# Kernel tuning notes

Measured on AMD Instinct MI355X. Metric: run time of the kernel, lower is better.

## Reference

```python
import jax, jax.numpy as jnp
import numpy as np

P, N, D = 8, 1024, 768
H = 12
HS = D // H
SCALE = float(HS ** 0.5)  # NOTE: original multiplies by sqrt(head_size)


def setup_inputs() -> dict:
    key = jax.random.key(0)
    k1, k2, k3 = jax.random.split(key, 3)
    pixel_values = jax.random.normal(k1, (P, N, D), dtype=jnp.float32)
    attention_mask = jnp.zeros((P, 1, 1, N), dtype=jnp.float32)
    qkv_w = jax.random.normal(k2, (D, 3 * D), dtype=jnp.float32) * 0.02
    qkv_b = jnp.zeros((3 * D,), dtype=jnp.float32)
    proj_w = jax.random.normal(k3, (D, D), dtype=jnp.float32) * 0.02
    proj_b = jnp.zeros((D,), dtype=jnp.float32)
    return {
        "pixel_values": pixel_values,
        "attention_mask": attention_mask,
        "qkv_w": qkv_w,
        "qkv_b": qkv_b,
        "proj_w": proj_w,
        "proj_b": proj_b,
    }


def reference(pixel_values, attention_mask, qkv_w, qkv_b, proj_w, proj_b):
    p, n, d = pixel_values.shape
    # fused QKV projection: (p, n, 3d) -> (3, p, H, n, hs)
    mixed = pixel_values @ qkv_w + qkv_b
    mixed = mixed.reshape(p, n, 3, H, HS).transpose(2, 0, 3, 1, 4)
    q, k, v = mixed[0], mixed[1], mixed[2]
    # scores: (p, H, n, n); original multiplies by sqrt(head_size)
    scores = jnp.einsum("phqd,phkd->phqk", q, k) * SCALE
    probs = jax.nn.softmax(scores, axis=-1)
    # dropout p=0 (identity in eval); mask added POST-softmax, per source
    probs = probs + attention_mask
    ctx = jnp.einsum("phqk,phkd->phqd", probs, v)
    ctx = ctx.transpose(0, 2, 1, 3).reshape(p, n, d)
    out = ctx @ proj_w + proj_b
    return out
```

## Files before the change

### kernel.cpp

```cpp
#include <hip/hip_runtime.h>
#include <hip/hip_bf16.h>
#include <cstdint>
#include <math.h>

constexpr int PB = 8;
constexpr int NS = 1024;
constexpr int DM = 768;
constexpr int NH = 12;
constexpr int HSZ = 64;
constexpr float QS    = 11.541560327111707f;
constexpr float EOFFL = 126.95716359822878f;

typedef short    bf16x8 __attribute__((ext_vector_type(8)));
typedef _Float16 half8  __attribute__((ext_vector_type(8)));
typedef __fp16   fp16x2 __attribute__((ext_vector_type(2)));
typedef float    floatx4 __attribute__((ext_vector_type(4)));

#if __has_builtin(__builtin_amdgcn_exp2f)
#define EXP2(x) __builtin_amdgcn_exp2f(x)
#else
#define EXP2(x) exp2f(x)
#endif

__device__ __forceinline__ ushort f2h(float x) {
    _Float16 h = (_Float16)x;
    return *reinterpret_cast<ushort*>(&h);
}
__device__ __forceinline__ float h2f(ushort u) {
    _Float16 h = __builtin_bit_cast(_Float16, u);
    return (float)h;
}
__device__ __forceinline__ ushort f2bf(float x) {
    __hip_bfloat16 b = __float2bfloat16(x);
    return *reinterpret_cast<ushort*>(&b);
}
__device__ __forceinline__ float bf2f(ushort u) {
    __hip_bfloat16 b = *reinterpret_cast<__hip_bfloat16*>(&u);
    return __bfloat162float(b);
}
__device__ __forceinline__ unsigned int pk2h(float a, float b) {
    fp16x2 h = __builtin_amdgcn_cvt_pkrtz(a, b);
    return __builtin_bit_cast(unsigned int, h);
}

#define GLDS(g, l)                                                             \
    __builtin_amdgcn_global_load_lds(                                          \
        (const __attribute__((address_space(1))) void*)(g),                    \
        (__attribute__((address_space(3))) void*)(l), 16, 0, 0)

__global__ void prep_kernel(const float* __restrict__ x, ushort* __restrict__ hf,
                            int n4,
                            const float* __restrict__ qkv_w, ushort* __restrict__ qwf,
                            const float* __restrict__ proj_w, ushort* __restrict__ pwf)
{
    const int bid = blockIdx.x;
    if (bid < 2048) {
        int i = bid * blockDim.x + threadIdx.x;
        const int stride = 2048 * blockDim.x;
        for (; i < n4; i += stride) {
            const float4 v = ((const float4*)x)[i];
            ((ushort4*)hf)[i] = ushort4{f2h(v.x), f2h(v.y), f2h(v.z), f2h(v.w)};
        }
        return;
    }
    __shared__ float tile[32][33];
    const int t  = threadIdx.x;
    const int tx = t & 31, ty = t >> 5;
    const float* w;
    ushort* fT;
    int bx, by, K, N;
    if (bid < 2048 + 1728) {
        const int id = bid - 2048;
        bx = id % 72; by = id / 72;
        w = qkv_w; fT = qwf; K = DM; N = 3 * DM;
    } else {
        const int id = bid - (2048 + 1728);
        bx = id % 24; by = id / 24;
        w = proj_w; fT = pwf; K = DM; N = DM;
    }
    #pragma unroll
    for (int r = 0; r < 4; ++r)
        tile[ty + r*8][tx] = w[(size_t)(by*32 + ty + r*8) * N + bx*32 + tx];
    __syncthreads();
    #pragma unroll
    for (int r = 0; r < 4; ++r) {
        const int n = bx*32 + ty + r*8;
        const int k = by*32 + tx;
        fT[(size_t)n * K + k] = f2h(tile[tx][ty + r*8]);
    }
}

template <int MODE>
__global__ __launch_bounds__(256, 3)
void gemm_f16(const ushort* __restrict__ Af, const ushort* __restrict__ Bf,
              const float* __restrict__ bias, float* __restrict__ outf,
              ushort* __restrict__ qf, ushort* __restrict__ kf,
              ushort* __restrict__ vt, int K)
{
    __shared__ __align__(16) ushort As[128*64];
    __shared__ __align__(16) ushort Bs[128*64];

    const int t    = threadIdx.x;
    const int w    = t >> 6;
    const int lane = t & 63;
    const int l15  = lane & 15;
    const int quad = lane >> 4;
    const int wm = w >> 1, wn = w & 1;
    const int m0 = blockIdx.x * 128, n0 = blockIdx.y * 128;

    floatx4 acc[4][4];
    #pragma unroll
    for (int i = 0; i < 4; ++i)
        #pragma unroll
        for (int j = 0; j < 4; ++j) acc[i][j] = floatx4{0.f, 0.f, 0.f, 0.f};

    const int srow8 = lane >> 3;
    const int sslot = lane & 7;

    for (int k0 = 0; k0 < K; k0 += 64) {
        #pragma unroll
        for (int j = 0; j < 4; ++j) {
            const int row = w*32 + j*8 + srow8;
            const int seg = sslot ^ (row & 7);
            const int ldst = (w*32 + j*8) * 64;
            GLDS(Af + (size_t)(m0 + row) * K + k0 + seg*8, As + ldst);
            GLDS(Bf + (size_t)(n0 + row) * K + k0 + seg*8, Bs + ldst);
        }
        __syncthreads();

        #pragma unroll
        for (int h2 = 0; h2 < 2; ++h2) {
            half8 fa[4], fb[4];
            #pragma unroll
            for (int i = 0; i < 4; ++i) {
                const int sl = ((h2*4 + quad) ^ (l15 & 7)) * 8;
                fa[i] = *(const half8*)(As + (wm*64 + i*16 + l15) * 64 + sl);
                fb[i] = *(const half8*)(Bs + (wn*64 + i*16 + l15) * 64 + sl);
            }
            #pragma unroll
            for (int mt = 0; mt < 4; ++mt)
                #pragma unroll
                for (int nt = 0; nt < 4; ++nt)
                    acc[mt][nt] = __builtin_amdgcn_mfma_f32_16x16x32_f16(fa[mt], fb[nt], acc[mt][nt], 0, 0, 0);
        }
        __syncthreads();
    }

    if (MODE == 0) {
        #pragma unroll
        for (int nt = 0; nt < 4; ++nt) {
            const int col = n0 + wn*64 + nt*16 + l15;
            const float bval = bias[col];
            #pragma unroll
            for (int mt = 0; mt < 4; ++mt) {
                const int row0 = m0 + wm*64 + mt*16 + quad*4;
                #pragma unroll
                for (int r = 0; r < 4; ++r)
                    outf[(size_t)(row0 + r) * DM + col] = acc[mt][nt][r] + bval;
            }
        }
    } else {
        const int jbase = n0 + wn*64;
        const int c  = jbase / DM;
        const int hh = (jbase % DM) >> 6;
        const int pp = (m0 + wm*64) >> 10;
        const size_t head = (size_t)pp * NH + hh;
        if (c < 2) {
            ushort* dst = (c == 0 ? qf : kf);
            const float qscale = (c == 0) ? QS : 1.0f;
            #pragma unroll
            for (int nt = 0; nt < 4; ++nt) {
                const int s = nt*16 + l15;
                const float bval = bias[jbase + s];
                #pragma unroll
                for (int mt = 0; mt < 4; ++mt) {
                    const int tok0 = m0 + wm*64 + mt*16 + quad*4;
                    const int nn0  = tok0 & 1023;
                    #pragma unroll
                    for (int r = 0; r < 4; ++r)
                        dst[(head*NS + nn0 + r) * HSZ + s] = f2h((acc[mt][nt][r] + bval) * qscale);
                }
            }
        } else {
            #pragma unroll
            for (int nt = 0; nt < 4; ++nt) {
                const int s = nt*16 + l15;
                const float bval = bias[jbase + s];
                #pragma unroll
                for (int mt = 0; mt < 4; ++mt) {
                    const int tok0 = m0 + wm*64 + mt*16 + quad*4;
                    const int nn0  = tok0 & 1023;
                    ushort4 pk;
                    pk.x = f2bf(acc[mt][nt][0] + bval);
                    pk.y = f2bf(acc[mt][nt][1] + bval);
                    pk.z = f2bf(acc[mt][nt][2] + bval);
                    pk.w = f2bf(acc[mt][nt][3] + bval);
                    *(ushort4*)(vt + (head*HSZ + s) * NS + nn0) = pk;
                }
            }
        }
    }
}

__global__ void mv_kernel(const float* __restrict__ mask, const ushort* __restrict__ vt,
                          float* __restrict__ mv)
{
    __shared__ float red[4][64];
    const int ph = blockIdx.x;
    const int t  = threadIdx.x;
    const int c  = t & 63, part = t >> 6;
    const ushort* vrow = vt + ((size_t)ph * HSZ + c) * NS + part * 256;
    const float*  mrow = mask + (size_t)(ph / NH) * NS + part * 256;
    float acc = 0.f;
    for (int k = 0; k < 256; k += 4) {
        const ushort4 v4 = *(const ushort4*)(vrow + k);
        const float4  m4 = *(const float4*)(mrow + k);
        acc += m4.x * bf2f(v4.x) + m4.y * bf2f(v4.y)
             + m4.z * bf2f(v4.z) + m4.w * bf2f(v4.w);
    }
    red[part][c] = acc;
    __syncthreads();
    if (t < 64)
        mv[(size_t)ph * HSZ + t] = red[0][t] + red[1][t] + red[2][t] + red[3][t];
}

__global__ __launch_bounds__(256, 3)
void attn_mfma_kernel(const ushort* __restrict__ qf, const ushort* __restrict__ kf,
                      const ushort* __restrict__ vt, const float* __restrict__ mv,
                      ushort* __restrict__ ctx)
{
    __shared__ __align__(16) ushort khs[2][64*64];
    __shared__ __align__(16) ushort vs [2][64*64];

    const int t    = threadIdx.x;
    const int w    = t >> 6;
    const int lane = t & 63;
    const int l15  = lane & 15;
    const int quad = lane >> 4;
    const int ph = blockIdx.x, qt = blockIdx.y;
    const int h  = ph % NH,    p  = ph / NH;
    const size_t headoff = ((size_t)p * NH + h) * (size_t)(NS * HSZ);

    const ushort* qpa = qf + headoff + (size_t)(qt*128 + w*16 + l15) * HSZ + quad*8;
    const half8 qa0 = *(const half8*)(qpa);
    const half8 qa1 = *(const half8*)(qpa + 32);
    const ushort* qpb = qpa + (size_t)64 * HSZ;
    const half8 qb0 = *(const half8*)(qpb);
    const half8 qb1 = *(const half8*)(qpb + 32);

    floatx4 oA[4], oB[4];
    float lsumA = 0.f, lsumB = 0.f;
    #pragma unroll
    for (int tc = 0; tc < 4; ++tc) {
        oA[tc] = floatx4{0.f, 0.f, 0.f, 0.f};
        oB[tc] = floatx4{0.f, 0.f, 0.f, 0.f};
    }

    const int srow8 = lane >> 3;
    const int sslot = lane & 7;
    const int xs = l15 & 7;

    auto stage = [&](int kt, int b) {
        #pragma unroll
        for (int j = 0; j < 2; ++j) {
            const int row  = w*16 + j*8 + srow8;
            const int segK = sslot ^ ((row & 3) | (((row >> 3) & 1) << 2));
            const int segV = sslot ^ (row & 7);
            const size_t gk = headoff + (size_t)(kt*64 + row) * HSZ + segK*8;
            const size_t gv = headoff + (size_t)row * NS + kt*64 + segV*8;
            const int ldst = (w*16 + j*8) * 64;
            GLDS(kf + gk, &khs[b][ldst]);
            GLDS(vt + gv, &vs [b][ldst]);
        }
    };

    stage(0, 0);
    int cur = 0;

    for (int kt = 0; kt < 16; ++kt) {
        __syncthreads();
        if (kt + 1 < 16) stage(kt + 1, cur ^ 1);

        const ushort* kbuf = khs[cur];
        const ushort* vbuf = vs [cur];

        bf16x8 bpA[2], bpB[2];
        #pragma unroll
        for (int tt = 0; tt < 4; ++tt) {
            const int rho = ((l15 >> 2) << 3) + ((tt & 1) << 2) + (l15 & 3) + ((tt >> 1) << 5);
            const int a0 = rho*64 + ((quad       ^ xs) * 8);
            const int a1 = rho*64 + (((quad | 4) ^ xs) * 8);
            const half8 bh0 = *(const half8*)(kbuf + a0);
            const half8 bh1 = *(const half8*)(kbuf + a1);
            floatx4 sA = floatx4{-EOFFL, -EOFFL, -EOFFL, -EOFFL};
            sA = __builtin_amdgcn_mfma_f32_16x16x32_f16(bh0, qa0, sA, 0, 0, 0);
            sA = __builtin_amdgcn_mfma_f32_16x16x32_f16(bh1, qa1, sA, 0, 0, 0);
            floatx4 sB = floatx4{-EOFFL, -EOFFL, -EOFFL, -EOFFL};
            sB = __builtin_amdgcn_mfma_f32_16x16x32_f16(bh0, qb0, sB, 0, 0, 0);
            sB = __builtin_amdgcn_mfma_f32_16x16x32_f16(bh1, qb1, sB, 0, 0, 0);
            const float a0e = EXP2(sA[0]);
            const float a1e = EXP2(sA[1]);
            const float a2e = EXP2(sA[2]);
            const float a3e = EXP2(sA[3]);
            lsumA += (a0e + a1e) + (a2e + a3e);
            const float b0e = EXP2(sB[0]);
            const float b1e = EXP2(sB[1]);
            const float b2e = EXP2(sB[2]);
            const float b3e = EXP2(sB[3]);
            lsumB += (b0e + b1e) + (b2e + b3e);
            const int off = (tt & 1) * 4;
            bf16x8& dA = bpA[tt >> 1];
            dA[off + 0] = (short)f2bf(a0e);
            dA[off + 1] = (short)f2bf(a1e);
            dA[off + 2] = (short)f2bf(a2e);
            dA[off + 3] = (short)f2bf(a3e);
            bf16x8& dB = bpB[tt >> 1];
            dB[off + 0] = (short)f2bf(b0e);
            dB[off + 1] = (short)f2bf(b1e);
            dB[off + 2] = (short)f2bf(b2e);
            dB[off + 3] = (short)f2bf(b3e);
        }

        #pragma unroll
        for (int tc = 0; tc < 4; ++tc) {
            const int crow = (tc*16 + l15) * 64;
            const bf16x8 va0 = *(const bf16x8*)(vbuf + crow + ((quad       ^ xs) * 8));
            const bf16x8 va1 = *(const bf16x8*)(vbuf + crow + (((quad | 4) ^ xs) * 8));
            oA[tc] = __builtin_amdgcn_mfma_f32_16x16x32_bf16(va0, bpA[0], oA[tc], 0, 0, 0);
            oA[tc] = __builtin_amdgcn_mfma_f32_16x16x32_bf16(va1, bpA[1], oA[tc], 0, 0, 0);
            oB[tc] = __builtin_amdgcn_mfma_f32_16x16x32_bf16(va0, bpB[0], oB[tc], 0, 0, 0);
            oB[tc] = __builtin_amdgcn_mfma_f32_16x16x32_bf16(va1, bpB[1], oB[tc], 0, 0, 0);
        }
        cur ^= 1;
    }

    float lA = lsumA;
    lA += __shfl_xor(lA, 16);
    lA += __shfl_xor(lA, 32);
    const float invA = 1.0f / lA;
    float lB = lsumB;
    lB += __shfl_xor(lB, 16);
    lB += __shfl_xor(lB, 32);
    const float invB = 1.0f / lB;

    const float* mvp = mv + ((size_t)p * NH + h) * HSZ;
    const int rowA = qt*128 + w*16 + l15;
    const size_t baseA = ((size_t)p * NS + rowA) * DM + h * 64;
    const size_t baseB = baseA + (size_t)64 * DM;
    #pragma unroll
    for (int tc = 0; tc < 4; ++tc) {
        const int c0 = tc*16 + quad*4;
        const float m0v = mvp[c0 + 0], m1v = mvp[c0 + 1];
        const float m2v = mvp[c0 + 2], m3v = mvp[c0 + 3];
        uint2 stA;
        stA.x = pk2h(oA[tc][0] * invA + m0v, oA[tc][1] * invA + m1v);
        stA.y = pk2h(oA[tc][2] * invA + m2v, oA[tc][3] * invA + m3v);
        *(uint2*)(ctx + baseA + c0) = stA;
        uint2 stB;
        stB.x = pk2h(oB[tc][0] * invB + m0v, oB[tc][1] * invB + m1v);
        stB.y = pk2h(oB[tc][2] * invB + m2v, oB[tc][3] * invB + m3v);
        *(uint2*)(ctx + baseB + c0) = stB;
    }
}

extern "C" void kernel_launch(void* const* d_in, const int* in_sizes, int n_in,
                              void* d_out, int out_size, void* d_ws, size_t ws_size,
                              hipStream_t stream)
{
    const float* x      = (const float*)d_in[0];
    const float* mask   = (const float*)d_in[1];
    const float* qkv_w  = (const float*)d_in[2];
    const float* qkv_b  = (const float*)d_in[3];
    const float* proj_w = (const float*)d_in[4];
    const float* proj_b = (const float*)d_in[5];
    float* out = (float*)d_out;

    const size_t HE = (size_t)PB * NH * NS * HSZ;
    const size_t QW = (size_t)DM * 3 * DM;
    const size_t PW = (size_t)DM * DM;
    ushort* xf  = (ushort*)d_ws;
    ushort* qwf = xf + HE;
    ushort* pwf = qwf + QW;
    ushort* qfv = pwf + PW;
    ushort* kfv = qfv + HE;
    ushort* vtv = kfv + HE;
    float*  mvb = (float*)(vtv + HE);
    ushort* cth = xf;

    prep_kernel<<<2048 + 1728 + 576, 256, 0, stream>>>(
        x, xf, (int)(HE / 4), qkv_w, qwf, proj_w, pwf);

    gemm_f16<1><<<dim3(PB*NS/128, 3*DM/128), 256, 0, stream>>>(
        xf, qwf, qkv_b, nullptr, qfv, kfv, vtv, DM);

    mv_kernel<<<dim3(PB*NH), 256, 0, stream>>>(mask, vtv, mvb);

    attn_mfma_kernel<<<dim3(PB*NH, NS/128), 256, 0, stream>>>(
        qfv, kfv, vtv, mvb, cth);

    gemm_f16<0><<<dim3(PB*NS/128, DM/128), 256, 0, stream>>>(
        cth, pwf, proj_b, out, nullptr, nullptr, nullptr, DM);
}
```

Baseline: 190.8 us.

## Double-buffer GEMM LDS tiles with 32-wide K steps to overlap loads

Rewrites the f16 GEMM main loop to use two 128x32 LDS buffers per operand. The global-to-LDS load of the next K slice is issued before the MFMAs on the current slice, and the second barrier per iteration is gone. The aim is to hide global load latency behind compute at the same LDS footprint. In exchange the K step halves, so there are twice as many iterations and barriers, and the swizzle now uses 4 segments, which may raise LDS bank conflicts.

```diff
diff --git a/kernel.cpp b/kernel.cpp
--- a/kernel.cpp
+++ b/kernel.cpp
@@ -97,8 +97,8 @@
               ushort* __restrict__ qf, ushort* __restrict__ kf,
               ushort* __restrict__ vt, int K)
 {
-    __shared__ __align__(16) ushort As[128*64];
-    __shared__ __align__(16) ushort Bs[128*64];
+    __shared__ __align__(16) ushort As[2][128*32];
+    __shared__ __align__(16) ushort Bs[2][128*32];
 
     const int t    = threadIdx.x;
     const int w    = t >> 6;
@@ -114,36 +114,42 @@
         #pragma unroll
         for (int j = 0; j < 4; ++j) acc[i][j] = floatx4{0.f, 0.f, 0.f, 0.f};
 
-    const int srow8 = lane >> 3;
-    const int sslot = lane & 7;
-
-    for (int k0 = 0; k0 < K; k0 += 64) {
-        #pragma unroll
-        for (int j = 0; j < 4; ++j) {
-            const int row = w*32 + j*8 + srow8;
-            const int seg = sslot ^ (row & 7);
-            const int ldst = (w*32 + j*8) * 64;
-            GLDS(Af + (size_t)(m0 + row) * K + k0 + seg*8, As + ldst);
-            GLDS(Bf + (size_t)(n0 + row) * K + k0 + seg*8, Bs + ldst);
-        }
+    const int srow = w*16 + (lane >> 2);
+    const int sseg = lane & 3;
+    const int nsteps = K >> 5;
+
+    auto stage = [&](int ks, int b) {
+        const int k0 = ks * 32;
+        #pragma unroll
+        for (int j = 0; j < 2; ++j) {
+            const int row = j*64 + srow;
+            const int ss  = sseg ^ (row & 3);
+            const int ldb = (j*64 + w*16) * 32;
+            GLDS(Af + (size_t)(m0 + row) * K + k0 + ss*8, &As[b][ldb]);
+            GLDS(Bf + (size_t)(n0 + row) * K + k0 + ss*8, &Bs[b][ldb]);
+        }
+    };
+
+    stage(0, 0);
+    int cur = 0;
+    const int rslot = (quad ^ (l15 & 3)) * 8;
+
+    for (int ks = 0; ks < nsteps; ++ks) {
         __syncthreads();
-
-        #pragma unroll
-        for (int h2 = 0; h2 < 2; ++h2) {
-            half8 fa[4], fb[4];
+        if (ks + 1 < nsteps) stage(ks + 1, cur ^ 1);
+
+        half8 fa[4], fb[4];
+        #pragma unroll
+        for (int i = 0; i < 4; ++i) {
+            fa[i] = *(const half8*)(&As[cur][(wm*64 + i*16 + l15) * 32 + rslot]);
+            fb[i] = *(const half8*)(&Bs[cur][(wn*64 + i*16 + l15) * 32 + rslot]);
+        }
+        #pragma unroll
+        for (int mt = 0; mt < 4; ++mt)
             #pragma unroll
-            for (int i = 0; i < 4; ++i) {
-                const int sl = ((h2*4 + quad) ^ (l15 & 7)) * 8;
-                fa[i] = *(const half8*)(As + (wm*64 + i*16 + l15) * 64 + sl);
-                fb[i] = *(const half8*)(Bs + (wn*64 + i*16 + l15) * 64 + sl);
-            }
-            #pragma unroll
-            for (int mt = 0; mt < 4; ++mt)
-                #pragma unroll
-                for (int nt = 0; nt < 4; ++nt)
-                    acc[mt][nt] = __builtin_amdgcn_mfma_f32_16x16x32_f16(fa[mt], fb[nt], acc[mt][nt], 0, 0, 0);
-        }
-        __syncthreads();
+            for (int nt = 0; nt < 4; ++nt)
+                acc[mt][nt] = __builtin_amdgcn_mfma_f32_16x16x32_f16(fa[mt], fb[nt], acc[mt][nt], 0, 0, 0);
+        cur ^= 1;
     }
 
     if (MODE == 0) {
```

Result: slower. 198.5 us (+4.0%).
